# Optimization experiments

Measured on AMD Instinct MI355X. Metric: run time of the kernel, lower is better.

The kernel has to match this reference:

```python
import jax, jax.numpy as jnp
import numpy as np

NEG_SLOPE = 0.2
HEADS = 8

def _gat_conv(x, src, dst, n_nodes, W, att_src, att_dst, bias):
    # x: [N, Fin], W: [Fin, H*C], att_*: [H, C], bias: [C]
    H, C = att_src.shape
    xl = (x @ W).reshape(n_nodes, H, C)                      # [N,H,C]
    a_src = (xl * att_src[None]).sum(-1)                      # [N,H]
    a_dst = (xl * att_dst[None]).sum(-1)                      # [N,H]
    e = jax.nn.leaky_relu(a_src[src] + a_dst[dst], NEG_SLOPE) # [E,H]
    m = jax.ops.segment_max(e, dst, num_segments=n_nodes)     # [N,H]
    ee = jnp.exp(e - m[dst])
    s = jax.ops.segment_sum(ee, dst, num_segments=n_nodes)    # [N,H]
    alpha = ee / s[dst]                                       # [E,H]
    msg = alpha[:, :, None] * xl[src]                         # [E,H,C]
    out = jax.ops.segment_sum(msg, dst, num_segments=n_nodes) # [N,H,C]
    return out.mean(axis=1) + bias                            # [N,C] (concat=False)

def setup_inputs() -> dict:
    key = jax.random.key(0)
    ks = jax.random.split(key, 12)
    N, E, EL = 50000, 800000, 200000
    V, D, HID, OUT = 5000, 128, 32, 32
    inp = {}
    inp['x'] = jax.random.randint(ks[0], (N,), 0, V)
    inp['edge_index'] = jax.random.randint(ks[1], (2, E), 0, N)
    inp['edge_label_index'] = jax.random.randint(ks[2], (2, EL), 0, N)
    inp['emb'] = jax.random.normal(ks[3], (V, D), jnp.float32) * D ** -0.5
    inp['W1'] = jax.random.normal(ks[4], (D, HEADS * HID), jnp.float32) * D ** -0.5
    inp['att_src1'] = jax.random.normal(ks[5], (HEADS, HID), jnp.float32) * HID ** -0.5
    inp['att_dst1'] = jax.random.normal(ks[6], (HEADS, HID), jnp.float32) * HID ** -0.5
    inp['b1'] = jnp.zeros((HID,), jnp.float32)
    inp['W2'] = jax.random.normal(ks[7], (HID, HEADS * OUT), jnp.float32) * HID ** -0.5
    inp['att_src2'] = jax.random.normal(ks[8], (HEADS, OUT), jnp.float32) * OUT ** -0.5
    inp['att_dst2'] = jax.random.normal(ks[9], (HEADS, OUT), jnp.float32) * OUT ** -0.5
    inp['b2'] = jnp.zeros((OUT,), jnp.float32)
    return inp

def reference(x, edge_index, edge_label_index, emb, W1, att_src1, att_dst1, b1, W2, att_src2, att_dst2, b2):
    N = x.shape[0]
    # PyG GATConv adds self-loops by default
    loop = jnp.arange(N)
    src = jnp.concatenate([edge_index[0], loop])
    dst = jnp.concatenate([edge_index[1], loop])
    h = emb[x]                                                   # [N, D] embedding lookup (squeeze(1) equivalent)
    h = jax.nn.relu(_gat_conv(h, src, dst, N, W1, att_src1, att_dst1, b1))
    # dropout p=0.5 is identity at inference (training=False)
    z = _gat_conv(h, src, dst, N, W2, att_src2, att_dst2, b2)    # [N, OUT]
    # decode: dot product over label edges
    return (z[edge_label_index[0]] * z[edge_label_index[1]]).sum(axis=-1)
```

## Files before the change

kernel.cpp:

```cpp
#include <hip/hip_runtime.h>
#include <hip/hip_fp16.h>
#include <math.h>
#include <limits.h>

#define HH 8
#define CC 32
#define NEG 0.2f

struct __align__(8) half4 { __half2 a, b; };

__device__ __forceinline__ void edge_sd(const int* __restrict__ ei, int e, int E, int& s, int& d){
  if(e < E){ s = ei[e]; d = ei[E+e]; } else { s = e-E; d = s; }
}


__global__ void k_zero(int* __restrict__ p, int n){
  int i = blockIdx.x*blockDim.x + threadIdx.x;
  if(i < n) p[i] = 0;
}

__global__ void k_count(const int* __restrict__ ei, int E, int ET, int* __restrict__ cnt){
  int e = blockIdx.x*blockDim.x + threadIdx.x;
  if(e >= ET) return;
  int d = (e < E) ? ei[E+e] : e-E;
  atomicAdd(&cnt[d], 1);
}

__global__ __launch_bounds__(256) void k_scan_block(const int* __restrict__ cnt,
                                                    int* __restrict__ off,
                                                    int* __restrict__ bsum, int N){
  int i = blockIdx.x*256 + threadIdx.x;
  int v = (i < N) ? cnt[i] : 0;
  int lane = threadIdx.x & 63;
  int incl = v;
  #pragma unroll
  for(int o=1;o<64;o<<=1){ int u = __shfl_up(incl,o); if(lane>=o) incl += u; }
  __shared__ int wsum[4];
  if(lane==63) wsum[threadIdx.x>>6] = incl;
  __syncthreads();
  int w = threadIdx.x>>6, wadd = 0;
  #pragma unroll
  for(int k=0;k<4;k++) if(k<w) wadd += wsum[k];
  if(i < N) off[i] = wadd + incl - v;
  if(threadIdx.x==255) bsum[blockIdx.x] = wadd + incl;
}

__global__ __launch_bounds__(256) void k_scan_bsum(int* __restrict__ bsum, int nb,
                                                   int* __restrict__ offN){
  int t = threadIdx.x;
  int v = (t < nb) ? bsum[t] : 0;
  int lane = t & 63;
  int incl = v;
  #pragma unroll
  for(int o=1;o<64;o<<=1){ int u = __shfl_up(incl,o); if(lane>=o) incl += u; }
  __shared__ int wsum[4];
  if(lane==63) wsum[t>>6] = incl;
  __syncthreads();
  int w = t>>6, wadd = 0;
  #pragma unroll
  for(int k=0;k<4;k++) if(k<w) wadd += wsum[k];
  if(t < nb) bsum[t] = wadd + incl - v;
  if(t == 255) *offN = wadd + incl;
}

__global__ void k_scan_add(int* __restrict__ off, const int* __restrict__ bsum,
                           int* __restrict__ cur, int N){
  int i = blockIdx.x*256 + threadIdx.x;
  if(i < N){ int v = off[i] + bsum[blockIdx.x]; off[i] = v; cur[i] = v; }
}

__global__ void k_scatter(const int* __restrict__ ei, int E, int ET,
                          const int* __restrict__ x,
                          int* __restrict__ cur, int* __restrict__ csr_src,
                          int* __restrict__ csr_xv){
  int e = blockIdx.x*blockDim.x + threadIdx.x;
  if(e >= ET) return;
  int s,d; edge_sd(ei,e,E,s,d);
  int pos = atomicAdd(&cur[d], 1);
  csr_src[pos] = s;
  csr_xv[pos]  = x[s];
}

__global__ __launch_bounds__(256) void k_ws(const float* __restrict__ W2,
                                            const float* __restrict__ att_s2,
                                            const float* __restrict__ att_d2,
                                            float* __restrict__ ws_s, float* __restrict__ ws_d){
  int k = threadIdx.x >> 3, h = threadIdx.x & 7;
  float ss = 0.f, dd = 0.f;
  for(int c=0;c<CC;c++){
    float w = W2[k*256 + h*CC + c];
    ss = fmaf(w, att_s2[h*CC+c], ss);
    dd = fmaf(w, att_d2[h*CC+c], dd);
  }
  ws_s[k*HH+h] = ss;
  ws_d[k*HH+h] = dd;
}

__global__ __launch_bounds__(256,4) void k_gemm1(
    const float* __restrict__ X, const float* __restrict__ W,
    const float* __restrict__ att_s, const float* __restrict__ att_d,
    __half* __restrict__ xl, float* __restrict__ a_src, float* __restrict__ a_dst, int V){
  const int ROWS = 8, FIN = 128;
  __shared__ __align__(16) float xs[ROWS][FIN];
  int row0 = blockIdx.x*ROWS;
  int tid = threadIdx.x;
  for(int p = tid; p < ROWS*FIN; p += 256){
    int r = p/FIN, kk = p - r*FIN;
    int row = row0 + r;
    xs[r][kk] = (row < V) ? X[(size_t)row*FIN + kk] : 0.f;
  }
  __syncthreads();
  float acc[ROWS];
  #pragma unroll
  for(int r=0;r<ROWS;r++) acc[r]=0.f;
  for(int k=0;k<FIN;k++){
    float w = W[(size_t)k*256 + tid];
    #pragma unroll
    for(int r=0;r<ROWS;r++) acc[r] = fmaf(xs[r][k], w, acc[r]);
  }
  float as = att_s[tid], ad = att_d[tid];
  #pragma unroll
  for(int r=0;r<ROWS;r++){
    int n = row0+r;
    float v = acc[r];
    float ps = v*as, pd = v*ad;
    #pragma unroll
    for(int msk=16; msk>=1; msk>>=1){
      ps += __shfl_xor(ps, msk);
      pd += __shfl_xor(pd, msk);
    }
    if(n < V){
      xl[(size_t)n*256 + tid] = __float2half(v);
      if((tid&31)==0){
        int hh = tid>>5;
        a_src[n*HH+hh] = ps;
        a_dst[n*HH+hh] = pd;
      }
    }
  }
}

__global__ __launch_bounds__(256) void k_fused1(
    const int* __restrict__ off, const int* __restrict__ csr_xv,
    const int* __restrict__ x,
    const float* __restrict__ a_src_v, const float* __restrict__ a_dst_v,
    const __half* __restrict__ xl_v, const float* __restrict__ bias,
    const float* __restrict__ ws_s, const float* __restrict__ ws_d,
    __half* __restrict__ h2h, float* __restrict__ a_src2, float* __restrict__ a_dst2, int N){
  int wid = (int)((blockIdx.x*(size_t)blockDim.x + threadIdx.x) >> 6);
  int lane = threadIdx.x & 63;
  if(wid >= N) return;
  const int start = off[wid], end = off[wid+1];
  const int t = lane >> 3, h = lane & 7;
  const int xv_n = x[wid];
  const float ad = a_dst_v[xv_n*HH + h];

  float m = -INFINITY;
  for(int j0 = start; j0 < end; j0 += 8){
    int jj = j0 + t;
    if(jj < end){
      float v = a_src_v[csr_xv[jj]*HH + h] + ad;
      v = v > 0.f ? v : NEG*v;
      m = fmaxf(m, v);
    }
  }
  #pragma unroll
  for(int msk=8; msk<64; msk<<=1) m = fmaxf(m, __shfl_xor(m, msk));

  const int h2 = lane >> 3, c0 = (lane & 7)*4;
  const __half* xp = xl_v + h2*CC + c0;
  float eesum = 0.f;
  float4 acc = make_float4(0.f,0.f,0.f,0.f);
  for(int j0 = start; j0 < end; j0 += 8){
    int jj = j0 + t;
    int sv = 0;
    float ee = 0.f;
    if(jj < end){
      sv = csr_xv[jj];
      float v = a_src_v[sv*HH + h] + ad;
      v = v > 0.f ? v : NEG*v;
      ee = expf(v - m);
      eesum += ee;
    }
    #pragma unroll
    for(int u=0; u<8; ++u){
      float a  = __shfl(ee, u*8 + h2);
      int   ss = __shfl(sv, u*8);
      half4 hv = *reinterpret_cast<const half4*>(xp + (size_t)ss*256);
      float2 f01 = __half22float2(hv.a), f23 = __half22float2(hv.b);
      acc.x = fmaf(a, f01.x, acc.x);
      acc.y = fmaf(a, f01.y, acc.y);
      acc.z = fmaf(a, f23.x, acc.z);
      acc.w = fmaf(a, f23.y, acc.w);
    }
  }
  #pragma unroll
  for(int msk=8; msk<64; msk<<=1) eesum += __shfl_xor(eesum, msk);
  float is2 = 0.125f / __shfl(eesum, h2);
  acc.x *= is2; acc.y *= is2; acc.z *= is2; acc.w *= is2;
  #pragma unroll
  for(int msk=8; msk<64; msk<<=1){
    acc.x += __shfl_xor(acc.x, msk);
    acc.y += __shfl_xor(acc.y, msk);
    acc.z += __shfl_xor(acc.z, msk);
    acc.w += __shfl_xor(acc.w, msk);
  }
  if(lane < 8){
    const float4 b = *reinterpret_cast<const float4*>(bias + c0);
    float4 o = make_float4(fmaxf(acc.x+b.x,0.f), fmaxf(acc.y+b.y,0.f),
                           fmaxf(acc.z+b.z,0.f), fmaxf(acc.w+b.w,0.f));
    half4 hv;
    hv.a = __floats2half2_rn(o.x, o.y);
    hv.b = __floats2half2_rn(o.z, o.w);
    *reinterpret_cast<half4*>(h2h + (size_t)wid*CC + c0) = hv;
    float ps = 0.f, pd = 0.f;
    #pragma unroll
    for(int g=0; g<8; ++g){
      float v0 = __shfl(o.x, g), v1 = __shfl(o.y, g), v2 = __shfl(o.z, g), v3 = __shfl(o.w, g);
      int kb = g*4;
      ps = fmaf(v0, ws_s[(kb+0)*HH+lane], ps);
      ps = fmaf(v1, ws_s[(kb+1)*HH+lane], ps);
      ps = fmaf(v2, ws_s[(kb+2)*HH+lane], ps);
      ps = fmaf(v3, ws_s[(kb+3)*HH+lane], ps);
      pd = fmaf(v0, ws_d[(kb+0)*HH+lane], pd);
      pd = fmaf(v1, ws_d[(kb+1)*HH+lane], pd);
      pd = fmaf(v2, ws_d[(kb+2)*HH+lane], pd);
      pd = fmaf(v3, ws_d[(kb+3)*HH+lane], pd);
    }
    a_src2[wid*HH + lane] = ps;
    a_dst2[wid*HH + lane] = pd;
  }
}

__global__ __launch_bounds__(256) void k_fused2(
    const int* __restrict__ off, const int* __restrict__ csr_src,
    const float* __restrict__ a_src2, const float* __restrict__ a_dst2,
    const __half* __restrict__ h2h, const float* __restrict__ W2,
    const float* __restrict__ b2, float* __restrict__ z, int N){
  __shared__ __align__(16) float aggl[4][256];
  int w = threadIdx.x >> 6;
  int wid = (int)(blockIdx.x*4 + w);
  int lane = threadIdx.x & 63;
  bool active = wid < N;
  int start = 0, end = 0;
  const int t = lane >> 3, h = lane & 7;
  float ad = 0.f;
  if(active){
    start = off[wid]; end = off[wid+1];
    ad = a_dst2[wid*HH + h];
  }

  float m = -INFINITY;
  for(int j0 = start; j0 < end; j0 += 8){
    int jj = j0 + t;
    if(jj < end){
      float v = a_src2[csr_src[jj]*HH + h] + ad;
      v = v > 0.f ? v : NEG*v;
      m = fmaxf(m, v);
    }
  }
  #pragma unroll
  for(int msk=8; msk<64; msk<<=1) m = fmaxf(m, __shfl_xor(m, msk));

  const int h2 = lane >> 3, k0 = (lane & 7)*4;
  const __half* hp = h2h + k0;
  float eesum = 0.f;
  float4 acc = make_float4(0.f,0.f,0.f,0.f);
  for(int j0 = start; j0 < end; j0 += 8){
    int jj = j0 + t;
    int s = 0;
    float ee = 0.f;
    if(jj < end){
      s = csr_src[jj];
      float v = a_src2[s*HH + h] + ad;
      v = v > 0.f ? v : NEG*v;
      ee = expf(v - m);
      eesum += ee;
    }
    #pragma unroll
    for(int u=0; u<8; ++u){
      float a  = __shfl(ee, u*8 + h2);
      int   ss = __shfl(s,  u*8);
      half4 hv = *reinterpret_cast<const half4*>(hp + (size_t)ss*CC);
      float2 f01 = __half22float2(hv.a), f23 = __half22float2(hv.b);
      acc.x = fmaf(a, f01.x, acc.x);
      acc.y = fmaf(a, f01.y, acc.y);
      acc.z = fmaf(a, f23.x, acc.z);
      acc.w = fmaf(a, f23.y, acc.w);
    }
  }
  #pragma unroll
  for(int msk=8; msk<64; msk<<=1) eesum += __shfl_xor(eesum, msk);
  float is2 = 0.125f / __shfl(eesum, h2);
  *reinterpret_cast<float4*>(&aggl[w][h2*CC + k0]) =
      make_float4(acc.x*is2, acc.y*is2, acc.z*is2, acc.w*is2);
  __syncthreads();

  const int ch = lane & 31, part = lane >> 5;
  float p = 0.f;
  #pragma unroll
  for(int hh = 0; hh < 4; ++hh){
    int hq = part*4 + hh;
    const float* wcol = W2 + hq*CC + ch;
    const float* arow = &aggl[w][hq*CC];
    #pragma unroll 8
    for(int k=0;k<CC;k++) p = fmaf(arow[k], wcol[(size_t)k*256], p);
  }
  p += __shfl_xor(p, 32);
  if(active && part==0) z[(size_t)wid*CC + ch] = p + b2[ch];
}

__global__ void k_decode(const int* __restrict__ eli, int EL,
                         const float* __restrict__ z, float* __restrict__ out){
  int e = blockIdx.x*blockDim.x + threadIdx.x;
  if(e >= EL) return;
  const float4* za = reinterpret_cast<const float4*>(z + (size_t)eli[e]*CC);
  const float4* zb = reinterpret_cast<const float4*>(z + (size_t)eli[EL+e]*CC);
  float s = 0.f;
  #pragma unroll
  for(int j=0;j<8;j++){
    float4 u = za[j], v = zb[j];
    s += u.x*v.x + u.y*v.y + u.z*v.z + u.w*v.w;
  }
  out[e] = s;
}

extern "C" void kernel_launch(void* const* d_in, const int* in_sizes, int n_in,
                              void* d_out, int out_size, void* d_ws, size_t ws_size,
                              hipStream_t stream){
  const int*   x   = (const int*)d_in[0];
  const int*   ei  = (const int*)d_in[1];
  const int*   eli = (const int*)d_in[2];
  const float* emb = (const float*)d_in[3];
  const float* W1  = (const float*)d_in[4];
  const float* as1 = (const float*)d_in[5];
  const float* ad1 = (const float*)d_in[6];
  const float* b1  = (const float*)d_in[7];
  const float* W2  = (const float*)d_in[8];
  const float* as2 = (const float*)d_in[9];
  const float* ad2 = (const float*)d_in[10];
  const float* b2  = (const float*)d_in[11];

  const int N  = in_sizes[0];
  const int V  = in_sizes[3]/128;
  const int E  = in_sizes[1]/2;
  const int EL = in_sizes[2]/2;
  const int ET = E + N;

  __half* xl_v = (__half*)d_ws;
  __half* h2h  = xl_v + (size_t)V*256;
  float* a_src_v = (float*)(h2h + (size_t)N*CC);
  float* a_dst_v = a_src_v + (size_t)V*HH;
  float* a_src2  = a_dst_v + (size_t)V*HH;
  float* a_dst2  = a_src2 + (size_t)N*HH;
  float* z       = a_dst2 + (size_t)N*HH;
  float* ws_s    = z + (size_t)N*CC;
  float* ws_d    = ws_s + 256;
  int*   cnt   = (int*)(ws_d + 256);
  int*   off   = cnt + N;
  int*   cur   = off + N + 1;
  int*   bsum  = cur + N;
  int*   csr   = bsum + ((N+255)/256);
  int*   csr_xv= csr + ET;

  dim3 blk(256);
  auto cdiv = [](long long a, long long b){ return (unsigned)((a+b-1)/b); };
  const int nb = (int)cdiv(N,256);

  k_zero<<<cdiv(N,256), blk, 0, stream>>>(cnt, N);
  k_count<<<cdiv(ET,256), blk, 0, stream>>>(ei, E, ET, cnt);
  k_scan_block<<<nb, blk, 0, stream>>>(cnt, off, bsum, N);
  k_scan_bsum<<<1, blk, 0, stream>>>(bsum, nb, off + N);
  k_scan_add<<<nb, blk, 0, stream>>>(off, bsum, cur, N);
  k_scatter<<<cdiv(ET,256), blk, 0, stream>>>(ei, E, ET, x, cur, csr, csr_xv);

  k_ws<<<1, blk, 0, stream>>>(W2, as2, ad2, ws_s, ws_d);

  k_gemm1<<<cdiv(V,8), blk, 0, stream>>>(emb, W1, as1, ad1, xl_v, a_src_v, a_dst_v, V);
  k_fused1<<<cdiv((long long)N*64,256), blk, 0, stream>>>(off, csr_xv, x, a_src_v, a_dst_v,
                                                          xl_v, b1, ws_s, ws_d,
                                                          h2h, a_src2, a_dst2, N);

  k_fused2<<<cdiv((long long)N*64,256), blk, 0, stream>>>(off, csr, a_src2, a_dst2,
                                                          h2h, W2, b2, z, N);

  k_decode<<<cdiv(EL,256), blk, 0, stream>>>(eli, EL, z, (float*)d_out);
}
```

Baseline: 326.2 us.

## Precompute edge attention scores in separate edge-parallel kernels before aggregation

Adds a k_score kernel that computes leaky-ReLU attention logits for every CSR edge and head in an edge-parallel pass, storing them contiguously. To support it, the scatter also writes csr_dst, and a small kernel gathers the per-node a_dst. The aggregation kernels then read scores with coalesced loads for both the max and exp passes, and batch the source-index loads 64 at a time. W2 is also pre-transposed so the final projection in fused2 uses float4 reads. This adds extra kernels and an ET*8 float score buffer written and re-read per layer, in exchange for removing dependent random gathers from the per-node loops.

After: 456.4 us. 39.9% more time.

```diff
diff --git a/kernel.cpp b/kernel.cpp
--- a/kernel.cpp
+++ b/kernel.cpp
@@ -72,13 +72,14 @@
 __global__ void k_scatter(const int* __restrict__ ei, int E, int ET,
                           const int* __restrict__ x,
                           int* __restrict__ cur, int* __restrict__ csr_src,
-                          int* __restrict__ csr_xv){
+                          int* __restrict__ csr_xv, int* __restrict__ csr_dst){
   int e = blockIdx.x*blockDim.x + threadIdx.x;
   if(e >= ET) return;
   int s,d; edge_sd(ei,e,E,s,d);
   int pos = atomicAdd(&cur[d], 1);
   csr_src[pos] = s;
   csr_xv[pos]  = x[s];
+  csr_dst[pos] = d;
 }
 
 __global__ __launch_bounds__(256) void k_ws(const float* __restrict__ W2,
@@ -94,6 +95,30 @@
   }
   ws_s[k*HH+h] = ss;
   ws_d[k*HH+h] = dd;
+}
+
+__global__ void k_w2t(const float* __restrict__ W2, float* __restrict__ W2t){
+  int i = blockIdx.x*256 + threadIdx.x;
+  if(i >= 8192) return;
+  int hc = i>>5, k = i&31;
+  W2t[i] = W2[k*256 + hc];
+}
+
+__global__ void k_adst1(const int* __restrict__ x, const float* __restrict__ a_dst_v,
+                        float* __restrict__ adst1, int N8){
+  int i = blockIdx.x*256 + threadIdx.x;
+  if(i >= N8) return;
+  adst1[i] = a_dst_v[x[i>>3]*HH + (i&7)];
+}
+
+__global__ void k_score(const int* __restrict__ sidx, const int* __restrict__ csr_dst,
+                        const float* __restrict__ asrc, const float* __restrict__ adstN,
+                        float* __restrict__ sc, int ET8){
+  int i = blockIdx.x*256 + threadIdx.x;
+  if(i >= ET8) return;
+  int j = i>>3, h = i&7;
+  float v = asrc[sidx[j]*HH + h] + adstN[csr_dst[j]*HH + h];
+  sc[i] = v > 0.f ? v : NEG*v;
 }
 
 __global__ __launch_bounds__(256,4) void k_gemm1(
@@ -142,56 +167,45 @@
 
 __global__ __launch_bounds__(256) void k_fused1(
     const int* __restrict__ off, const int* __restrict__ csr_xv,
-    const int* __restrict__ x,
-    const float* __restrict__ a_src_v, const float* __restrict__ a_dst_v,
-    const __half* __restrict__ xl_v, const float* __restrict__ bias,
+    const float* __restrict__ sc, const __half* __restrict__ xl_v,
+    const float* __restrict__ bias,
     const float* __restrict__ ws_s, const float* __restrict__ ws_d,
     __half* __restrict__ h2h, float* __restrict__ a_src2, float* __restrict__ a_dst2, int N){
   int wid = (int)((blockIdx.x*(size_t)blockDim.x + threadIdx.x) >> 6);
   int lane = threadIdx.x & 63;
   if(wid >= N) return;
-  const int start = off[wid], end = off[wid+1];
+  const int start = off[wid], end = off[wid+1], deg = end - start;
+  const float* scn = sc + (size_t)start*HH;
+
+  float m = -INFINITY;
+  for(int p = lane; p < deg*HH; p += 64) m = fmaxf(m, scn[p]);
+  #pragma unroll
+  for(int msk=8; msk<64; msk<<=1) m = fmaxf(m, __shfl_xor(m, msk));
+
   const int t = lane >> 3, h = lane & 7;
-  const int xv_n = x[wid];
-  const float ad = a_dst_v[xv_n*HH + h];
-
-  float m = -INFINITY;
-  for(int j0 = start; j0 < end; j0 += 8){
-    int jj = j0 + t;
-    if(jj < end){
-      float v = a_src_v[csr_xv[jj]*HH + h] + ad;
-      v = v > 0.f ? v : NEG*v;
-      m = fmaxf(m, v);
-    }
-  }
-  #pragma unroll
-  for(int msk=8; msk<64; msk<<=1) m = fmaxf(m, __shfl_xor(m, msk));
-
   const int h2 = lane >> 3, c0 = (lane & 7)*4;
   const __half* xp = xl_v + h2*CC + c0;
   float eesum = 0.f;
   float4 acc = make_float4(0.f,0.f,0.f,0.f);
-  for(int j0 = start; j0 < end; j0 += 8){
-    int jj = j0 + t;
-    int sv = 0;
-    float ee = 0.f;
-    if(jj < end){
-      sv = csr_xv[jj];
-      float v = a_src_v[sv*HH + h] + ad;
-      v = v > 0.f ? v : NEG*v;
-      ee = expf(v - m);
-      eesum += ee;
-    }
-    #pragma unroll
-    for(int u=0; u<8; ++u){
-      float a  = __shfl(ee, u*8 + h2);
-      int   ss = __shfl(sv, u*8);
-      half4 hv = *reinterpret_cast<const half4*>(xp + (size_t)ss*256);
-      float2 f01 = __half22float2(hv.a), f23 = __half22float2(hv.b);
-      acc.x = fmaf(a, f01.x, acc.x);
-      acc.y = fmaf(a, f01.y, acc.y);
-      acc.z = fmaf(a, f23.x, acc.z);
-      acc.w = fmaf(a, f23.y, acc.w);
+  for(int c = 0; c < deg; c += 64){
+    int el = csr_xv[start + min(c + lane, deg-1)];
+    int nb = min(64, deg - c);
+    for(int b = 0; b < nb; b += 8){
+      int jj = c + b + t;
+      float sv = scn[(size_t)(b + c)*HH + lane];
+      float ee = 0.f;
+      if(jj < deg){ ee = expf(sv - m); eesum += ee; }
+      #pragma unroll
+      for(int u=0; u<8; ++u){
+        float a  = __shfl(ee, u*8 + h2);
+        int   ss = __shfl(el, b + u);
+        half4 hv = *reinterpret_cast<const half4*>(xp + (size_t)ss*256);
+        float2 f01 = __half22float2(hv.a), f23 = __half22float2(hv.b);
+        acc.x = fmaf(a, f01.x, acc.x);
+        acc.y = fmaf(a, f01.y, acc.y);
+        acc.z = fmaf(a, f23.x, acc.z);
+        acc.w = fmaf(a, f23.y, acc.w);
+      }
     }
   }
   #pragma unroll
@@ -234,59 +248,48 @@
 
 __global__ __launch_bounds__(256) void k_fused2(
     const int* __restrict__ off, const int* __restrict__ csr_src,
-    const float* __restrict__ a_src2, const float* __restrict__ a_dst2,
-    const __half* __restrict__ h2h, const float* __restrict__ W2,
-    const float* __restrict__ b2, float* __restrict__ z, int N){
+    const float* __restrict__ sc, const __half* __restrict__ h2h,
+    const float* __restrict__ W2t, const float* __restrict__ b2,
+    float* __restrict__ z, int N){
   __shared__ __align__(16) float aggl[4][256];
   int w = threadIdx.x >> 6;
   int wid = (int)(blockIdx.x*4 + w);
   int lane = threadIdx.x & 63;
   bool active = wid < N;
   int start = 0, end = 0;
-  const int t = lane >> 3, h = lane & 7;
-  float ad = 0.f;
-  if(active){
-    start = off[wid]; end = off[wid+1];
-    ad = a_dst2[wid*HH + h];
-  }
+  if(active){ start = off[wid]; end = off[wid+1]; }
+  const int deg = end - start;
+  const float* scn = sc + (size_t)start*HH;
 
   float m = -INFINITY;
-  for(int j0 = start; j0 < end; j0 += 8){
-    int jj = j0 + t;
-    if(jj < end){
-      float v = a_src2[csr_src[jj]*HH + h] + ad;
-      v = v > 0.f ? v : NEG*v;
-      m = fmaxf(m, v);
-    }
-  }
+  for(int p = lane; p < deg*HH; p += 64) m = fmaxf(m, scn[p]);
   #pragma unroll
   for(int msk=8; msk<64; msk<<=1) m = fmaxf(m, __shfl_xor(m, msk));
 
+  const int t = lane >> 3;
   const int h2 = lane >> 3, k0 = (lane & 7)*4;
   const __half* hp = h2h + k0;
   float eesum = 0.f;
   float4 acc = make_float4(0.f,0.f,0.f,0.f);
-  for(int j0 = start; j0 < end; j0 += 8){
-    int jj = j0 + t;
-    int s = 0;
-    float ee = 0.f;
-    if(jj < end){
-      s = csr_src[jj];
-      float v = a_src2[s*HH + h] + ad;
-      v = v > 0.f ? v : NEG*v;
-      ee = expf(v - m);
-      eesum += ee;
-    }
-    #pragma unroll
-    for(int u=0; u<8; ++u){
-      float a  = __shfl(ee, u*8 + h2);
-      int   ss = __shfl(s,  u*8);
-      half4 hv = *reinterpret_cast<const half4*>(hp + (size_t)ss*CC);
-      float2 f01 = __half22float2(hv.a), f23 = __half22float2(hv.b);
-      acc.x = fmaf(a, f01.x, acc.x);
-      acc.y = fmaf(a, f01.y, acc.y);
-      acc.z = fmaf(a, f23.x, acc.z);
-      acc.w = fmaf(a, f23.y, acc.w);
+  for(int c = 0; c < deg; c += 64){
+    int el = csr_src[start + min(c + lane, deg-1)];
+    int nb = min(64, deg - c);
+    for(int b = 0; b < nb; b += 8){
+      int jj = c + b + t;
+      float sv = scn[(size_t)(b + c)*HH + lane];
+      float ee = 0.f;
+      if(jj < deg){ ee = expf(sv - m); eesum += ee; }
+      #pragma unroll
+      for(int u=0; u<8; ++u){
+        float a  = __shfl(ee, u*8 + h2);
+        int   ss = __shfl(el, b + u);
+        half4 hv = *reinterpret_cast<const half4*>(hp + (size_t)ss*CC);
+        float2 f01 = __half22float2(hv.a), f23 = __half22float2(hv.b);
+        acc.x = fmaf(a, f01.x, acc.x);
+        acc.y = fmaf(a, f01.y, acc.y);
+        acc.z = fmaf(a, f23.x, acc.z);
+        acc.w = fmaf(a, f23.y, acc.w);
+      }
     }
   }
   #pragma unroll
@@ -301,10 +304,16 @@
   #pragma unroll
   for(int hh = 0; hh < 4; ++hh){
     int hq = part*4 + hh;
-    const float* wcol = W2 + hq*CC + ch;
+    const float4* wrow = reinterpret_cast<const float4*>(W2t + ((size_t)hq*CC + ch)*CC);
     const float* arow = &aggl[w][hq*CC];
-    #pragma unroll 8
-    for(int k=0;k<CC;k++) p = fmaf(arow[k], wcol[(size_t)k*256], p);
+    #pragma unroll
+    for(int k4=0; k4<8; ++k4){
+      float4 wv = wrow[k4];
+      p = fmaf(arow[4*k4+0], wv.x, p);
+      p = fmaf(arow[4*k4+1], wv.y, p);
+      p = fmaf(arow[4*k4+2], wv.z, p);
+      p = fmaf(arow[4*k4+3], wv.w, p);
+    }
   }
   p += __shfl_xor(p, 32);
   if(active && part==0) z[(size_t)wid*CC + ch] = p + b2[ch];
@@ -351,17 +360,21 @@
   __half* h2h  = xl_v + (size_t)V*256;
   float* a_src_v = (float*)(h2h + (size_t)N*CC);
   float* a_dst_v = a_src_v + (size_t)V*HH;
-  float* a_src2  = a_dst_v + (size_t)V*HH;
+  float* adst1   = a_dst_v + (size_t)V*HH;
+  float* a_src2  = adst1 + (size_t)N*HH;
   float* a_dst2  = a_src2 + (size_t)N*HH;
   float* z       = a_dst2 + (size_t)N*HH;
-  float* ws_s    = z + (size_t)N*CC;
+  float* sc      = z + (size_t)N*CC;
+  float* ws_s    = sc + (size_t)ET*HH;
   float* ws_d    = ws_s + 256;
-  int*   cnt   = (int*)(ws_d + 256);
+  float* W2t     = ws_d + 256;
+  int*   cnt   = (int*)(W2t + 8192);
   int*   off   = cnt + N;
   int*   cur   = off + N + 1;
   int*   bsum  = cur + N;
   int*   csr   = bsum + ((N+255)/256);
   int*   csr_xv= csr + ET;
+  int*   csr_dst = csr_xv + ET;
 
   dim3 blk(256);
   auto cdiv = [](long long a, long long b){ return (unsigned)((a+b-1)/b); };
@@ -372,17 +385,19 @@
   k_scan_block<<<nb, blk, 0, stream>>>(cnt, off, bsum, N);
   k_scan_bsum<<<1, blk, 0, stream>>>(bsum, nb, off + N);
   k_scan_add<<<nb, blk, 0, stream>>>(off, bsum, cur, N);
-  k_scatter<<<cdiv(ET,256), blk, 0, stream>>>(ei, E, ET, x, cur, csr, csr_xv);
+  k_scatter<<<cdiv(ET,256), blk, 0, stream>>>(ei, E, ET, x, cur, csr, csr_xv, csr_dst);
 
   k_ws<<<1, blk, 0, stream>>>(W2, as2, ad2, ws_s, ws_d);
+  k_w2t<<<32, blk, 0, stream>>>(W2, W2t);
 
   k_gemm1<<<cdiv(V,8), blk, 0, stream>>>(emb, W1, as1, ad1, xl_v, a_src_v, a_dst_v, V);
-  k_fused1<<<cdiv((long long)N*64,256), blk, 0, stream>>>(off, csr_xv, x, a_src_v, a_dst_v,
-                                                          xl_v, b1, ws_s, ws_d,
-                                                          h2h, a_src2, a_dst2, N);
-
-  k_fused2<<<cdiv((long long)N*64,256), blk, 0, stream>>>(off, csr, a_src2, a_dst2,
-                                                          h2h, W2, b2, z, N);
+  k_adst1<<<cdiv((long long)N*HH,256), blk, 0, stream>>>(x, a_dst_v, adst1, N*HH);
+  k_score<<<cdiv((long long)ET*HH,256), blk, 0, stream>>>(csr_xv, csr_dst, a_src_v, adst1, sc, ET*HH);
+  k_fused1<<<cdiv((long long)N*64,256), blk, 0, stream>>>(off, csr_xv, sc, xl_v, b1,
+                                                          ws_s, ws_d, h2h, a_src2, a_dst2, N);
+
+  k_score<<<cdiv((long long)ET*HH,256), blk, 0, stream>>>(csr, csr_dst, a_src2, a_dst2, sc, ET*HH);
+  k_fused2<<<cdiv((long long)N*64,256), blk, 0, stream>>>(off, csr, sc, h2h, W2t, b2, z, N);
 
   k_decode<<<cdiv(EL,256), blk, 0, stream>>>(eli, EL, z, (float*)d_out);
 }
```
